# Kernel tuning notes

Measured on AMD Instinct MI355X. Metric: run time of the kernel, lower is better.

## Reference

```python
import jax, jax.numpy as jnp
import numpy as np

N = 10000; E = 320000
DIM = 176; ATT = 16; SH_HEADS = 16; TH = 4; NH = SH_HEADS + TH; VD = DIM // SH_HEADS
LMAX = 3; NSPH = (LMAX + 1) ** 2; ZDIM = 16; RDIM = 16
RSTART = 0.8; CUT = 5.0; NLAYERS = 2


def _ln(x):
    mu = jnp.mean(x, axis=-1, keepdims=True)
    dx = x - mu
    var = jnp.mean(dx ** 2, axis=-1, keepdims=True)
    return dx * (1e-6 + var) ** (-0.5)


def _sph(v):
    # real spherical harmonics up to l=3, unnormalized overall scale, [E,16]
    x, y, z = v[..., 0], v[..., 1], v[..., 2]
    s3 = np.float32(np.sqrt(3.0)); s15 = np.float32(np.sqrt(15.0))
    c1 = np.float32(np.sqrt(5.0 / 8.0)); c2 = np.float32(np.sqrt(3.0 / 8.0))
    x2, y2, z2 = x * x, y * y, z * z
    return jnp.stack([
        jnp.ones_like(x),
        x, y, z,
        s3 * x * y, s3 * y * z, 0.5 * (3.0 * z2 - 1.0), s3 * x * z, 0.5 * s3 * (x2 - y2),
        c1 * y * (3.0 * x2 - y2), s15 * x * y * z, c2 * y * (5.0 * z2 - 1.0),
        0.5 * z * (5.0 * z2 - 3.0), c2 * x * (5.0 * z2 - 1.0),
        0.5 * s15 * z * (x2 - y2), c1 * x * (x2 - 3.0 * y2),
    ], axis=-1)


def setup_inputs() -> dict:
    key = jax.random.key(0)
    ks = jax.random.split(key, 32)

    def rn(k, shape):
        fan_in = shape[0] if len(shape) > 1 else shape[0]
        return jax.random.normal(k, shape, dtype=jnp.float32) / np.float32(np.sqrt(shape[0]))

    species = jax.random.randint(ks[0], (N,), 0, 64)
    edge_src = jax.random.randint(ks[1], (E,), 0, N)
    edge_dst = jax.random.randint(ks[2], (E,), 0, N)
    distances = RSTART + (CUT - RSTART) * jax.random.uniform(ks[3], (E,), dtype=jnp.float32)
    raw = jax.random.normal(ks[4], (E, 3), dtype=jnp.float32)
    dirn = raw / jnp.linalg.norm(raw, axis=-1, keepdims=True)
    vec = dirn * distances[:, None]
    switch = 0.5 * (jnp.cos(jnp.pi * distances / CUT) + 1.0)

    inp = {
        'species': species, 'distances': distances, 'switch': switch,
        'edge_src': edge_src, 'edge_dst': edge_dst, 'vec': vec,
        'z_table': jax.random.normal(ks[5], (64, ZDIM), dtype=jnp.float32),
        'w_species': rn(ks[6], (ZDIM, DIM)),
        'pos_w1_0': rn(ks[7], (RDIM, 2 * ATT)), 'pos_b1_0': jnp.zeros((2 * ATT,), jnp.float32),
        'pos_w2_0': rn(ks[8], (2 * ATT, ATT)), 'pos_b2_0': jnp.zeros((ATT,), jnp.float32),
        'wq_0': rn(ks[9], (DIM, NH * ATT)), 'wk_0': rn(ks[10], (DIM, NH * ATT)),
        'wv_0': rn(ks[11], (DIM, SH_HEADS * VD)),
        'upd_w_0': rn(ks[12], (2 * DIM, DIM)), 'upd_b_0': jnp.zeros((DIM,), jnp.float32),
        'pos_w1_1': rn(ks[13], (RDIM + TH * (LMAX + 1), 2 * ATT)), 'pos_b1_1': jnp.zeros((2 * ATT,), jnp.float32),
        'pos_w2_1': rn(ks[14], (2 * ATT, ATT)), 'pos_b2_1': jnp.zeros((ATT,), jnp.float32),
        'wq_1': rn(ks[15], (DIM, NH * ATT)), 'wk_1': rn(ks[16], (DIM, NH * ATT)),
        'wv_1': rn(ks[17], (DIM, SH_HEADS * VD)),
        'upd_w_1': rn(ks[18], (2 * DIM, DIM)), 'upd_b_1': jnp.zeros((DIM,), jnp.float32),
    }
    return inp


def reference(species, distances, switch, edge_src, edge_dst, vec,
              z_table, w_species,
              pos_w1_0, pos_b1_0, pos_w2_0, pos_b2_0, wq_0, wk_0, wv_0, upd_w_0, upd_b_0,
              pos_w1_1, pos_b1_1, pos_w2_1, pos_b2_1, wq_1, wk_1, wv_1, upd_w_1, upd_b_1):
    Nn = species.shape[0]
    Zi = z_table[species]                      # [N, ZDIM] species encoding
    xi = _ln(Zi @ w_species)                   # [N, DIM]

    vhat = vec / distances[:, None]
    Yij = _sph(vhat)                           # [E, NSPH]
    ls = np.repeat(np.arange(LMAX + 1), 2 * np.arange(LMAX + 1) + 1)
    parity = jnp.asarray(((-1.0) ** ls).astype(np.float32))  # [NSPH]

    centers = jnp.linspace(RSTART, CUT, RDIM, dtype=jnp.float32)
    sigma = np.float32((CUT - RSTART) / (RDIM - 1))
    radial = jnp.exp(-(((distances[:, None] - centers) / sigma) ** 2))  # [E, RDIM]

    Vi = jnp.zeros((Nn, TH, NSPH), jnp.float32)
    pos = [(pos_w1_0, pos_b1_0, pos_w2_0, pos_b2_0), (pos_w1_1, pos_b1_1, pos_w2_1, pos_b2_1)]
    att = [(wq_0, wk_0, wv_0, upd_w_0, upd_b_0), (wq_1, wk_1, wv_1, upd_w_1, upd_b_1)]
    inv_sqrt_d = np.float32(1.0 / np.sqrt(ATT))

    for layer in range(NLAYERS):
        pw1, pb1, pw2, pb2 = pos[layer]
        wq, wk, wv, uw, ub = att[layer]
        if layer == 0:
            ur = radial
        else:
            # tensor relative positional features: [E, TH, NSPH]
            xij2 = (Vi[edge_dst] + (parity * Vi)[edge_src]) * Yij[:, None, :]
            us = [xij2[:, :, l * l:(l + 1) * (l + 1)].sum(axis=-1) for l in range(LMAX + 1)]
            ur = jnp.concatenate([radial] + us, axis=-1)
        w = jax.nn.swish(ur @ pw1 + pb1) @ pw2 + pb2     # [E, ATT] positional encoding
        q = (xi @ wq).reshape(Nn, NH, ATT)
        k = (xi @ wk).reshape(Nn, NH, ATT)
        # multiplicative relative positional attention coefficients [E, NH]
        aij = jnp.einsum('ehd,ed->eh', q[edge_dst] * k[edge_src], w) * (switch[:, None] * inv_sqrt_d)
        a_s, a_t = aij[:, :SH_HEADS], aij[:, SH_HEADS:]
        v = (xi @ wv).reshape(Nn, SH_HEADS, VD)
        mi = jax.ops.segment_sum(a_s[:, :, None] * v[edge_src], edge_dst, num_segments=Nn)  # [N,SH,VD]
        Vi = Vi + jax.ops.segment_sum(
            a_t[:, :, None] * (Yij[:, None, :] + parity * Vi[edge_src]), edge_dst, num_segments=Nn)
        ui = jnp.concatenate([xi, mi.reshape(Nn, -1)], axis=-1)
        xi = _ln(xi + ui @ uw + ub)
    return xi
```

## Files before the change

### kernel.cpp

```cpp
#include <hip/hip_runtime.h>
#include <hip/hip_bf16.h>
#include <math.h>

#define N_NODES 10000
#define N_PAD   10048
#define N_EDGES 320000
#define DIM     176
#define ATT     16
#define SH_HEADS 16
#define THH     4
#define NH      20
#define VD      11
#define ZDIM    16
#define RDIM    16
#define QK_W    (NH*ATT)
#define QKV_W   816
#define UI_W    (2*DIM)
#define KQ      192
#define SIGINV  3.5714285714285716f
#define RSTEP   0.28f

typedef unsigned short ushort_t;
typedef __attribute__((ext_vector_type(8))) short bf16x8;
typedef __attribute__((ext_vector_type(4))) float f32x4;


__device__ __forceinline__ ushort_t f2bf(float f) {
    __hip_bfloat16 b = __float2bfloat16(f);
    return *(ushort_t*)&b;
}

__device__ __forceinline__ float bf2f(ushort_t u) {
    return __uint_as_float(((unsigned)u) << 16);
}

__device__ __forceinline__ void sph16(float x, float y, float z, float* Y) {
    const float s3  = 1.7320508075688772f;
    const float s15 = 3.872983346207417f;
    const float c1  = 0.7905694150420949f;
    const float c2  = 0.6123724356957945f;
    float x2 = x*x, y2 = y*y, z2 = z*z;
    Y[0]  = 1.0f;
    Y[1]  = x;
    Y[2]  = y;
    Y[3]  = z;
    Y[4]  = s3 * x * y;
    Y[5]  = s3 * y * z;
    Y[6]  = 0.5f * (3.0f * z2 - 1.0f);
    Y[7]  = s3 * x * z;
    Y[8]  = 0.5f * s3 * (x2 - y2);
    Y[9]  = c1 * y * (3.0f * x2 - y2);
    Y[10] = s15 * x * y * z;
    Y[11] = c2 * y * (5.0f * z2 - 1.0f);
    Y[12] = 0.5f * z * (5.0f * z2 - 3.0f);
    Y[13] = c2 * x * (5.0f * z2 - 1.0f);
    Y[14] = 0.5f * s15 * z * (x2 - y2);
    Y[15] = c1 * x * (x2 - 3.0f * y2);
}

__device__ __forceinline__ void unpack8(const uint4 u, float* f) {
    f[0] = __uint_as_float(u.x << 16);
    f[1] = __uint_as_float(u.x & 0xffff0000u);
    f[2] = __uint_as_float(u.y << 16);
    f[3] = __uint_as_float(u.y & 0xffff0000u);
    f[4] = __uint_as_float(u.z << 16);
    f[5] = __uint_as_float(u.z & 0xffff0000u);
    f[6] = __uint_as_float(u.w << 16);
    f[7] = __uint_as_float(u.w & 0xffff0000u);
}


__global__ __launch_bounds__(256) void k_deg(const int* edst, int* deg) {
    int e = blockIdx.x * 256 + threadIdx.x;
    if (e < N_EDGES) atomicAdd(&deg[edst[e]], 1);
}

__global__ __launch_bounds__(1024) void k_scan1(const int* deg, int* incl, int* bsum) {
    __shared__ int sd[1024];
    int b = blockIdx.x, tid = threadIdx.x;
    int gi = b * 1024 + tid;
    int v = (gi < N_NODES) ? deg[gi] : 0;
    sd[tid] = v;
    __syncthreads();
    for (int s = 1; s < 1024; s <<= 1) {
        int add = (tid >= s) ? sd[tid - s] : 0;
        __syncthreads();
        sd[tid] += add;
        __syncthreads();
    }
    if (gi < N_NODES) incl[gi] = sd[tid];
    if (tid == 1023) bsum[b] = sd[1023];
}

__global__ __launch_bounds__(1024) void k_scan3(const int* deg, const int* incl, const int* bsum,
                                                int* off, int* cursor) {
    __shared__ int bpre_s;
    int b = blockIdx.x, tid = threadIdx.x;
    if (tid == 0) {
        int acc = 0;
        for (int k = 0; k < b; k++) acc += bsum[k];
        bpre_s = acc;
    }
    __syncthreads();
    int gi = b * 1024 + tid;
    if (gi < N_NODES) {
        int e = bpre_s + incl[gi];
        off[gi + 1] = e;
        cursor[gi]  = e - deg[gi];
    }
    if (gi == 0) off[0] = 0;
}

__global__ __launch_bounds__(256) void k_scatter_reorder(const int* esrc, const int* edst,
        const float* dist, const float* swit, const float* vec, int* cursor,
        int* src_c, int* dst_c, float* dist_c, float* sc_c, float* Yf) {
    int e = blockIdx.x * 256 + threadIdx.x;
    if (e >= N_EDGES) return;
    int t_ = edst[e];
    int p = atomicAdd(&cursor[t_], 1);
    float d = dist[e];
    float inv = 1.0f / d;
    float vx = vec[(size_t)e*3 + 0] * inv;
    float vy = vec[(size_t)e*3 + 1] * inv;
    float vz = vec[(size_t)e*3 + 2] * inv;
    src_c[p]  = esrc[e];
    dst_c[p]  = t_;
    dist_c[p] = d;
    sc_c[p]   = swit[e] * 0.25f;
    float Y[16];
    sph16(vx, vy, vz, Y);
    #pragma unroll
    for (int m = 0; m < 16; m += 4)
        *(float4*)&Yf[(size_t)p * 16 + m] = make_float4(Y[m], Y[m+1], Y[m+2], Y[m+3]);
}


__device__ __forceinline__ void prep_qkv_body(int bid, int tid, const float* wq,
        const float* wk, const float* wv, ushort_t* Wtq) {
    int id = bid * 256 + tid;
    if (id >= 832 * KQ) return;
    int n = id / KQ, k = id - (id / KQ) * KQ;
    float v = 0.0f;
    if (k < DIM && n < QKV_W)
        v = (n < 320) ? wq[k * 320 + n] : (n < 640) ? wk[k * 320 + (n - 320)]
                                                    : wv[k * DIM + (n - 640)];
    Wtq[id] = f2bf(v);
}

__device__ __forceinline__ void prep_upd_body(int bid, int tid, const float* uw, ushort_t* Wtu) {
    int id = bid * 256 + tid;
    if (id >= 192 * UI_W) return;
    int n = id / UI_W, k = id - (id / UI_W) * UI_W;
    float v = (n < DIM) ? uw[k * DIM + n] : 0.0f;
    Wtu[id] = f2bf(v);
}

__device__ __forceinline__ void prep_mlp_body(int bid, int tid, const float* pw1,
        const float* pw2, ushort_t* w1T, ushort_t* w2T, int K1) {
    int id = bid * 256 + tid;
    if (id < 1024) {
        int n = id >> 5, k = id & 31;
        w1T[n * 32 + k] = (k < K1) ? f2bf(pw1[k * 32 + n]) : 0;
    } else if (id < 1536) {
        int id2 = id - 1024;
        int n = id2 >> 5, k = id2 & 31;
        w2T[n * 32 + k] = f2bf(pw2[k * 16 + n]);
    }
}

__global__ __launch_bounds__(256) void k_prep_all(
        const float* wq0, const float* wk0, const float* wv0, ushort_t* Wtq0,
        const float* wq1, const float* wk1, const float* wv1, ushort_t* Wtq1,
        const float* uw0, ushort_t* Wtu0, const float* uw1, ushort_t* Wtu1,
        const float* pw1_0, const float* pw2_0, ushort_t* w1T0, ushort_t* w2T0,
        const float* pw1_1, const float* pw2_1, ushort_t* w1T1, ushort_t* w2T1) {
    int bid = blockIdx.x, tid = threadIdx.x;
    if (bid < 624)        prep_qkv_body(bid,        tid, wq0, wk0, wv0, Wtq0);
    else if (bid < 1248)  prep_qkv_body(bid - 624,  tid, wq1, wk1, wv1, Wtq1);
    else if (bid < 1512)  prep_upd_body(bid - 1248, tid, uw0, Wtu0);
    else if (bid < 1776)  prep_upd_body(bid - 1512, tid, uw1, Wtu1);
    else if (bid < 1782)  prep_mlp_body(bid - 1776, tid, pw1_0, pw2_0, w1T0, w2T0, 16);
    else if (bid < 1788)  prep_mlp_body(bid - 1782, tid, pw1_1, pw2_1, w1T1, w2T1, 32);
}


template<int KCHUNKS, int OMODE>
__global__ __launch_bounds__(256) void k_gemm(const ushort_t* __restrict__ A, int sA,
                                              const ushort_t* __restrict__ Bt, int sB,
                                              void* __restrict__ Cv, int sC, int M, int N,
                                              ushort_t* __restrict__ qh,
                                              ushort_t* __restrict__ kh,
                                              ushort_t* __restrict__ vh) {
    __shared__ ushort_t As[64 * 40];
    __shared__ ushort_t Bs[64 * 40];
    int tid  = threadIdx.x;
    int m0   = blockIdx.y * 64, n0 = blockIdx.x * 64;
    int w    = tid >> 6, lane = tid & 63, quad = lane >> 4, c16 = lane & 15;
    int arow = tid >> 2, aseg = tid & 3;
    f32x4 acc[4] = {};
    for (int kc = 0; kc < KCHUNKS; kc++) {
        int k0 = kc * 32;
        *(uint4*)&As[arow * 40 + aseg * 8] =
            *(const uint4*)&A[(size_t)(m0 + arow) * sA + k0 + aseg * 8];
        *(uint4*)&Bs[arow * 40 + aseg * 8] =
            *(const uint4*)&Bt[(size_t)(n0 + arow) * sB + k0 + aseg * 8];
        __syncthreads();
        bf16x8 a = *(const bf16x8*)&As[(w * 16 + c16) * 40 + quad * 8];
        #pragma unroll
        for (int t = 0; t < 4; t++) {
            bf16x8 b = *(const bf16x8*)&Bs[(t * 16 + c16) * 40 + quad * 8];
            acc[t] = __builtin_amdgcn_mfma_f32_16x16x32_bf16(a, b, acc[t], 0, 0, 0);
        }
        __syncthreads();
    }
    #pragma unroll
    for (int t = 0; t < 4; t++) {
        #pragma unroll
        for (int r = 0; r < 4; r++) {
            int row = m0 + w * 16 + quad * 4 + r;
            int col = n0 + t * 16 + c16;
            if (row < M && col < N) {
                if (OMODE == 1) {
                    ushort_t bv = f2bf(acc[t][r]);
                    if (col < 320)      qh[(size_t)row * QK_W + col] = bv;
                    else if (col < 640) kh[(size_t)row * QK_W + (col - 320)] = bv;
                    else                vh[(size_t)row * DIM  + (col - 640)] = bv;
                } else {
                    ((float*)Cv)[(size_t)row * sC + col] = acc[t][r];
                }
            }
        }
    }
}


__global__ __launch_bounds__(256) void k_node_init(const int* species, const float* z_table,
                                                   const float* wsp, float* xi,
                                                   ushort_t* xib, ushort_t* cxm) {
    __shared__ float zs[16 * ZDIM];
    __shared__ float yt[16 * DIM];
    __shared__ float red[256];
    __shared__ float mus[16], rstds[16];
    int base = blockIdx.x * 16;
    int tid  = threadIdx.x;
    { int n = tid >> 4, kk = tid & 15;
      zs[tid] = z_table[species[base + n] * ZDIM + kk]; }
    __syncthreads();
    int c = tid;
    if (c < DIM) {
        float acc[16];
        #pragma unroll
        for (int n = 0; n < 16; n++) acc[n] = 0.0f;
        for (int kk = 0; kk < ZDIM; kk++) {
            float w = wsp[kk * DIM + c];
            #pragma unroll
            for (int n = 0; n < 16; n++) acc[n] += zs[n * ZDIM + kk] * w;
        }
        #pragma unroll
        for (int n = 0; n < 16; n++) yt[n * DIM + c] = acc[n];
    }
    __syncthreads();
    { int n2 = tid >> 4, j = tid & 15;
      float s = 0.0f;
      for (int c2 = j; c2 < DIM; c2 += 16) s += yt[n2 * DIM + c2];
      red[tid] = s; }
    __syncthreads();
    if (tid < 16) { float s = 0; for (int j = 0; j < 16; j++) s += red[tid * 16 + j]; mus[tid] = s / (float)DIM; }
    __syncthreads();
    { int n2 = tid >> 4, j = tid & 15;
      float mu = mus[n2], s = 0.0f;
      for (int c2 = j; c2 < DIM; c2 += 16) { float d = yt[n2 * DIM + c2] - mu; s += d * d; }
      red[tid] = s; }
    __syncthreads();
    if (tid < 16) { float s = 0; for (int j = 0; j < 16; j++) s += red[tid * 16 + j]; rstds[tid] = rsqrtf(s / (float)DIM + 1e-6f); }
    __syncthreads();
    if (c < DIM) {
        #pragma unroll
        for (int n = 0; n < 16; n++) {
            float val = (yt[n * DIM + c] - mus[n]) * rstds[n];
            xi[(size_t)(base + n) * DIM + c] = val;
            ushort_t bv = f2bf(val);
            xib[(size_t)(base + n) * KQ + c]   = bv;
            cxm[(size_t)(base + n) * UI_W + c] = bv;
        }
    } else if (c < KQ) {
        #pragma unroll
        for (int n = 0; n < 16; n++) xib[(size_t)(base + n) * KQ + c] = 0;
    }
}


template<bool L0>
__global__ __launch_bounds__(256) void k_edge(const float* dist_c, const float* sc_c,
        const int* src_c, const int* dst_c, const float* Yf, const ushort_t* Vih,
        const ushort_t* qh, const ushort_t* kh,
        const ushort_t* w1T, const float* pb1, const ushort_t* w2T, const float* pb2,
        ushort_t* aijh) {
    __shared__ ushort_t urS[64 * 40];
    __shared__ ushort_t Ht[4][16 * 40];
    __shared__ float    wdS[64 * 17];
    __shared__ ushort_t aS[NH][64];
    int tid  = threadIdx.x;
    int w    = tid >> 6, lane = tid & 63, quad = lane >> 4, c16 = lane & 15;
    int eb   = blockIdx.x * 64;

    int le = tid >> 2, part = tid & 3;
    int ie = eb + le;
    int sE = src_c[ie], tE = dst_c[ie];

    if (!L0) {
        int e  = tid & 63, tp = tid >> 6;
        int i  = eb + e;
        float d = dist_c[i];
        ushort_t ur4[4];
        #pragma unroll
        for (int r0 = 0; r0 < 4; r0++) {
            int r = tp * 4 + r0;
            float cc = 0.8f + (float)r * RSTEP;
            float uu = (d - cc) * SIGINV;
            ur4[r0] = f2bf(__expf(-uu * uu));
        }
        *(uint2*)&urS[e * 40 + tp * 4] = *(uint2*)ur4;
        float Y[16];
        #pragma unroll
        for (int m = 0; m < 16; m += 4) {
            float4 y = *(const float4*)&Yf[(size_t)i * 16 + m];
            Y[m] = y.x; Y[m+1] = y.y; Y[m+2] = y.z; Y[m+3] = y.w;
        }
        int s = src_c[i], t_ = dst_c[i];
        const uint4* vd4 = (const uint4*)(Vih + (size_t)t_ * 64);
        const uint4* vs4 = (const uint4*)(Vih + (size_t)s  * 64);
        int th = tp;
        float fd[16], fs[16];
        unpack8(vd4[2*th],   fd);     unpack8(vd4[2*th+1], fd+8);
        unpack8(vs4[2*th],   fs);     unpack8(vs4[2*th+1], fs+8);
        float us0 = (fd[0] + fs[0]) * Y[0];
        float us1 = 0.0f, us2 = 0.0f, us3 = 0.0f;
        #pragma unroll
        for (int m = 1; m < 4; m++)  us1 += (fd[m] - fs[m]) * Y[m];
        #pragma unroll
        for (int m = 4; m < 9; m++)  us2 += (fd[m] + fs[m]) * Y[m];
        #pragma unroll
        for (int m = 9; m < 16; m++) us3 += (fd[m] - fs[m]) * Y[m];
        urS[e * 40 + 16 + 0 * 4 + th] = f2bf(us0);
        urS[e * 40 + 16 + 1 * 4 + th] = f2bf(us1);
        urS[e * 40 + 16 + 2 * 4 + th] = f2bf(us2);
        urS[e * 40 + 16 + 3 * 4 + th] = f2bf(us3);
        __syncthreads();
    }

    uint4 kr[10];
    {
        const uint4* kseg = (const uint4*)(kh + (size_t)sE * QK_W) + part * 10;
        #pragma unroll
        for (int j = 0; j < 10; j++) kr[j] = kseg[j];
    }

    {
        int e0 = eb + w * 16;
        bf16x8 a1;
        if (L0) {
            float d = dist_c[e0 + c16];
            #pragma unroll
            for (int j = 0; j < 8; j++) {
                int r = quad * 8 + j;
                float v = 0.0f;
                if (r < 16) { float cc = 0.8f + (float)r * RSTEP; float uu = (d - cc) * SIGINV; v = __expf(-uu * uu); }
                a1[j] = (short)f2bf(v);
            }
        } else {
            a1 = *(const bf16x8*)&urS[(w * 16 + c16) * 40 + quad * 8];
        }
        bf16x8 b0 = *(const bf16x8*)&w1T[c16 * 32 + quad * 8];
        bf16x8 b1 = *(const bf16x8*)&w1T[(16 + c16) * 32 + quad * 8];
        f32x4 acc0 = {}, acc1 = {};
        acc0 = __builtin_amdgcn_mfma_f32_16x16x32_bf16(a1, b0, acc0, 0, 0, 0);
        acc1 = __builtin_amdgcn_mfma_f32_16x16x32_bf16(a1, b1, acc1, 0, 0, 0);
        float bb0 = pb1[c16], bb1 = pb1[c16 + 16];
        #pragma unroll
        for (int r = 0; r < 4; r++) {
            int er = quad * 4 + r;
            float h0 = acc0[r] + bb0; h0 = h0 / (1.0f + __expf(-h0));
            float h1 = acc1[r] + bb1; h1 = h1 / (1.0f + __expf(-h1));
            Ht[w][er * 40 + c16]      = f2bf(h0);
            Ht[w][er * 40 + 16 + c16] = f2bf(h1);
        }
        __syncthreads();
        bf16x8 a2 = *(const bf16x8*)&Ht[w][c16 * 40 + quad * 8];
        bf16x8 b2 = *(const bf16x8*)&w2T[c16 * 32 + quad * 8];
        f32x4 acc2 = {};
        acc2 = __builtin_amdgcn_mfma_f32_16x16x32_bf16(a2, b2, acc2, 0, 0, 0);
        float bb2 = pb2[c16];
        #pragma unroll
        for (int r = 0; r < 4; r++) {
            int er = quad * 4 + r;
            wdS[(w * 16 + er) * 17 + c16] = (acc2[r] + bb2) * sc_c[e0 + er];
        }
    }
    __syncthreads();

    {
        float wd[16];
        #pragma unroll
        for (int p = 0; p < 16; p++) wd[p] = wdS[le * 17 + p];
        const uint4* q4 = (const uint4*)(qh + (size_t)tE * QK_W) + part * 10;
        #pragma unroll
        for (int j = 0; j < 5; j++) {
            int h = part * 5 + j;
            float qa[8], qb[8], ka[8], kb[8];
            unpack8(q4[2*j],   qa); unpack8(q4[2*j+1], qb);
            unpack8(kr[2*j],   ka); unpack8(kr[2*j+1], kb);
            float acc = 0.0f;
            #pragma unroll
            for (int dd = 0; dd < 8; dd++) acc += qa[dd] * ka[dd] * wd[dd];
            #pragma unroll
            for (int dd = 0; dd < 8; dd++) acc += qb[dd] * kb[dd] * wd[8 + dd];
            aS[h][le] = f2bf(acc);
        }
    }
    __syncthreads();
    {
        const uint* aSw = (const uint*)aS;
        for (int idx = tid; idx < NH * 32; idx += 256) {
            int h = idx >> 5, w2 = idx & 31;
            *(uint*)(aijh + (size_t)h * N_EDGES + eb + w2 * 2) = aSw[h * 32 + w2];
        }
    }
}


__device__ __forceinline__ void mi_step(int i, int c0, bool f1, bool f2,
        const int* src_c, const ushort_t* aA, const ushort_t* aB, const ushort_t* vh,
        float& acc0, float& acc1, float& acc2, float& acc3) {
    int s0 = src_c[i];
    uint2 v0 = *(const uint2*)(vh + (size_t)s0 * DIM + c0);
    float a00 = bf2f(aA[i]), a0B = bf2f(aB[i]);
    float g01 = f1 ? a0B : a00, g02 = f2 ? a0B : a00;
    acc0 += a00 * __uint_as_float(v0.x << 16);
    acc1 += g01 * __uint_as_float(v0.x & 0xffff0000u);
    acc2 += g02 * __uint_as_float(v0.y << 16);
    acc3 += a0B * __uint_as_float(v0.y & 0xffff0000u);
}

__device__ __forceinline__ void mi_wave(int n, int lane, const int* off, const int* src_c,
        const ushort_t* aijh, const ushort_t* vh, ushort_t* cxm) {
    if (lane >= 44) return;
    int c0 = lane * 4;
    int hA = c0 / VD;
    int hB = (c0 + 3) / VD;
    bool f1 = ((c0 + 1) / VD) != hA;
    bool f2 = ((c0 + 2) / VD) != hA;
    const ushort_t* aA = aijh + (size_t)hA * N_EDGES;
    const ushort_t* aB = aijh + (size_t)hB * N_EDGES;
    int start = off[n], end = off[n + 1];
    float acc0 = 0, acc1 = 0, acc2 = 0, acc3 = 0;
    int cnt = end - start;
    int i = start;

#define MI_ACC(vv, av, bv) { \
    float aa = bf2f(av), ab = bf2f(bv); \
    float g1 = f1 ? ab : aa, g2 = f2 ? ab : aa; \
    acc0 += aa * __uint_as_float((vv).x << 16); \
    acc1 += g1 * __uint_as_float((vv).x & 0xffff0000u); \
    acc2 += g2 * __uint_as_float((vv).y << 16); \
    acc3 += ab * __uint_as_float((vv).y & 0xffff0000u); }

    if (cnt >= 4) {
        int iend = start + (cnt & ~3);
        int s0 = src_c[i], s1 = src_c[i+1], s2 = src_c[i+2], s3 = src_c[i+3];
        uint2 v0 = *(const uint2*)(vh + (size_t)s0 * DIM + c0);
        uint2 v1 = *(const uint2*)(vh + (size_t)s1 * DIM + c0);
        uint2 v2 = *(const uint2*)(vh + (size_t)s2 * DIM + c0);
        uint2 v3 = *(const uint2*)(vh + (size_t)s3 * DIM + c0);
        ushort_t pA0 = aA[i], pA1 = aA[i+1], pA2 = aA[i+2], pA3 = aA[i+3];
        ushort_t pB0 = aB[i], pB1 = aB[i+1], pB2 = aB[i+2], pB3 = aB[i+3];
        for (i += 4; i + 4 <= iend; i += 4) {
            int t0 = src_c[i], t1 = src_c[i+1], t2 = src_c[i+2], t3 = src_c[i+3];
            uint2 w0 = *(const uint2*)(vh + (size_t)t0 * DIM + c0);
            uint2 w1 = *(const uint2*)(vh + (size_t)t1 * DIM + c0);
            uint2 w2 = *(const uint2*)(vh + (size_t)t2 * DIM + c0);
            uint2 w3 = *(const uint2*)(vh + (size_t)t3 * DIM + c0);
            ushort_t qA0 = aA[i], qA1 = aA[i+1], qA2 = aA[i+2], qA3 = aA[i+3];
            ushort_t qB0 = aB[i], qB1 = aB[i+1], qB2 = aB[i+2], qB3 = aB[i+3];
            MI_ACC(v0, pA0, pB0); MI_ACC(v1, pA1, pB1);
            MI_ACC(v2, pA2, pB2); MI_ACC(v3, pA3, pB3);
            v0 = w0; v1 = w1; v2 = w2; v3 = w3;
            pA0 = qA0; pA1 = qA1; pA2 = qA2; pA3 = qA3;
            pB0 = qB0; pB1 = qB1; pB2 = qB2; pB3 = qB3;
        }
        MI_ACC(v0, pA0, pB0); MI_ACC(v1, pA1, pB1);
        MI_ACC(v2, pA2, pB2); MI_ACC(v3, pA3, pB3);
    }
    for (; i < end; i++)
        mi_step(i, c0, f1, f2, src_c, aA, aB, vh, acc0, acc1, acc2, acc3);
#undef MI_ACC
    ushort_t o[4] = {f2bf(acc0), f2bf(acc1), f2bf(acc2), f2bf(acc3)};
    *(uint2*)(cxm + (size_t)n * UI_W + DIM + c0) = *(uint2*)o;
}

__device__ __forceinline__ void vi_wave(int n, int lane, const int* off,
        const float* Yf, const ushort_t* aijh, ushort_t* Vih) {
    int th = lane >> 4, sm = lane & 15;
    const ushort_t* ah = aijh + (size_t)(SH_HEADS + th) * N_EDGES;
    int start = off[n], end = off[n + 1];
    float acc = 0.0f;
    int cnt = end - start;
    int i = start;
    if (cnt >= 4) {
        int iend = start + (cnt & ~3);
        float a0 = bf2f(ah[i]),   y0 = Yf[(size_t)i * 16 + sm];
        float a1 = bf2f(ah[i+1]), y1 = Yf[(size_t)(i+1) * 16 + sm];
        float a2 = bf2f(ah[i+2]), y2 = Yf[(size_t)(i+2) * 16 + sm];
        float a3 = bf2f(ah[i+3]), y3 = Yf[(size_t)(i+3) * 16 + sm];
        for (i += 4; i + 4 <= iend; i += 4) {
            float b0 = bf2f(ah[i]),   z0 = Yf[(size_t)i * 16 + sm];
            float b1 = bf2f(ah[i+1]), z1 = Yf[(size_t)(i+1) * 16 + sm];
            float b2 = bf2f(ah[i+2]), z2 = Yf[(size_t)(i+2) * 16 + sm];
            float b3 = bf2f(ah[i+3]), z3 = Yf[(size_t)(i+3) * 16 + sm];
            acc += a0 * y0 + a1 * y1 + a2 * y2 + a3 * y3;
            a0 = b0; a1 = b1; a2 = b2; a3 = b3;
            y0 = z0; y1 = z1; y2 = z2; y3 = z3;
        }
        acc += a0 * y0 + a1 * y1 + a2 * y2 + a3 * y3;
    }
    for (; i < end; i++)
        acc += bf2f(ah[i]) * Yf[(size_t)i * 16 + sm];
    Vih[(size_t)n * 64 + lane] = f2bf(acc);
}

__global__ __launch_bounds__(256) void k_agg0(const int* off, const int* src_c,
        const float* Yf, const ushort_t* aijh, const ushort_t* vh,
        ushort_t* cxm, ushort_t* Vih) {
    int wid  = blockIdx.x * 4 + (threadIdx.x >> 6);
    int lane = threadIdx.x & 63;
    if (wid < N_NODES)
        mi_wave(wid, lane, off, src_c, aijh, vh, cxm);
    else
        vi_wave(wid - N_NODES, lane, off, Yf, aijh, Vih);
}

__global__ __launch_bounds__(256) void k_agg1(const int* off, const int* src_c,
        const ushort_t* aijh, const ushort_t* vh, ushort_t* cxm) {
    int wid  = blockIdx.x * 4 + (threadIdx.x >> 6);
    int lane = threadIdx.x & 63;
    mi_wave(wid, lane, off, src_c, aijh, vh, cxm);
}


__global__ __launch_bounds__(256) void k_lnfinal(const float* yg, const float* xi,
        const float* ub, float* xo, ushort_t* xib, ushort_t* cxm) {
    __shared__ float yt[16 * DIM];
    __shared__ float red[256];
    __shared__ float mus[16], rstds[16];
    int base = blockIdx.x * 16;
    int tid  = threadIdx.x;
    for (int idx = tid; idx < 16 * DIM; idx += 256) {
        int n = idx / DIM, c = idx - n * DIM;
        yt[idx] = xi[(size_t)(base + n) * DIM + c]
                + yg[(size_t)(base + n) * DIM + c] + ub[c];
    }
    __syncthreads();
    { int n2 = tid >> 4, j = tid & 15;
      float s = 0.0f;
      for (int c2 = j; c2 < DIM; c2 += 16) s += yt[n2 * DIM + c2];
      red[tid] = s; }
    __syncthreads();
    if (tid < 16) { float s = 0; for (int j = 0; j < 16; j++) s += red[tid * 16 + j]; mus[tid] = s / (float)DIM; }
    __syncthreads();
    { int n2 = tid >> 4, j = tid & 15;
      float mu = mus[n2], s = 0.0f;
      for (int c2 = j; c2 < DIM; c2 += 16) { float d = yt[n2 * DIM + c2] - mu; s += d * d; }
      red[tid] = s; }
    __syncthreads();
    if (tid < 16) { float s = 0; for (int j = 0; j < 16; j++) s += red[tid * 16 + j]; rstds[tid] = rsqrtf(s / (float)DIM + 1e-6f); }
    __syncthreads();
    int c = tid;
    if (c < DIM) {
        #pragma unroll
        for (int n = 0; n < 16; n++) {
            float val = (yt[n * DIM + c] - mus[n]) * rstds[n];
            xo[(size_t)(base + n) * DIM + c] = val;
            ushort_t bv = f2bf(val);
            xib[(size_t)(base + n) * KQ + c]   = bv;
            cxm[(size_t)(base + n) * UI_W + c] = bv;
        }
    } else if (c < KQ) {
        #pragma unroll
        for (int n = 0; n < 16; n++) xib[(size_t)(base + n) * KQ + c] = 0;
    }
}


extern "C" void kernel_launch(void* const* d_in, const int* in_sizes, int n_in,
                              void* d_out, int out_size, void* d_ws, size_t ws_size,
                              hipStream_t stream) {
    const int*   species = (const int*)  d_in[0];
    const float* dist    = (const float*)d_in[1];
    const float* swit    = (const float*)d_in[2];
    const int*   esrc    = (const int*)  d_in[3];
    const int*   edst    = (const int*)  d_in[4];
    const float* vec     = (const float*)d_in[5];
    const float* z_table = (const float*)d_in[6];
    const float* wsp     = (const float*)d_in[7];
    const float* pw1_0 = (const float*)d_in[8],  *pb1_0 = (const float*)d_in[9];
    const float* pw2_0 = (const float*)d_in[10], *pb2_0 = (const float*)d_in[11];
    const float* wq0 = (const float*)d_in[12], *wk0 = (const float*)d_in[13];
    const float* wv0 = (const float*)d_in[14], *uw0 = (const float*)d_in[15];
    const float* ub0 = (const float*)d_in[16];
    const float* pw1_1 = (const float*)d_in[17], *pb1_1 = (const float*)d_in[18];
    const float* pw2_1 = (const float*)d_in[19], *pb2_1 = (const float*)d_in[20];
    const float* wq1 = (const float*)d_in[21], *wk1 = (const float*)d_in[22];
    const float* wv1 = (const float*)d_in[23], *uw1 = (const float*)d_in[24];
    const float* ub1 = (const float*)d_in[25];
    float* out = (float*)d_out;

    char* p = (char*)d_ws;
    auto alloc = [&](size_t bytes) -> char* {
        char* r = p;
        p += (bytes + 255) & ~(size_t)255;
        return r;
    };
    int* deg    = (int*)alloc((size_t)N_NODES * 4);
    int* incl   = (int*)alloc((size_t)N_NODES * 4);
    int* bsum   = (int*)alloc(64);
    int* off    = (int*)alloc((size_t)(N_NODES + 1) * 4);
    int* cursor = (int*)alloc((size_t)N_NODES * 4);
    int*   src_c  = (int*)  alloc((size_t)N_EDGES * 4);
    int*   dst_c  = (int*)  alloc((size_t)N_EDGES * 4);
    float* dist_c = (float*)alloc((size_t)N_EDGES * 4);
    float* sc_c   = (float*)alloc((size_t)N_EDGES * 4);
    float* Yf     = (float*)alloc((size_t)N_EDGES * 16 * 4);
    float* xiA  = (float*)alloc((size_t)N_NODES * DIM * 4);
    float* xiB  = (float*)alloc((size_t)N_NODES * DIM * 4);
    ushort_t* xib  = (ushort_t*)alloc((size_t)N_PAD * KQ * 2);
    ushort_t* cxm  = (ushort_t*)alloc((size_t)N_PAD * UI_W * 2);
    ushort_t* qh   = (ushort_t*)alloc((size_t)N_NODES * QK_W * 2);
    ushort_t* kh   = (ushort_t*)alloc((size_t)N_NODES * QK_W * 2);
    ushort_t* vh   = (ushort_t*)alloc((size_t)N_NODES * DIM * 2);
    float* ybuf    = (float*)alloc((size_t)N_NODES * DIM * 4);
    ushort_t* Wtq0 = (ushort_t*)alloc((size_t)832 * KQ * 2);
    ushort_t* Wtq1 = (ushort_t*)alloc((size_t)832 * KQ * 2);
    ushort_t* Wtu0 = (ushort_t*)alloc((size_t)192 * UI_W * 2);
    ushort_t* Wtu1 = (ushort_t*)alloc((size_t)192 * UI_W * 2);
    ushort_t* w1T0 = (ushort_t*)alloc((size_t)32 * 32 * 2);
    ushort_t* w2T0 = (ushort_t*)alloc((size_t)16 * 32 * 2);
    ushort_t* w1T1 = (ushort_t*)alloc((size_t)32 * 32 * 2);
    ushort_t* w2T1 = (ushort_t*)alloc((size_t)16 * 32 * 2);
    ushort_t* Vih  = (ushort_t*)alloc((size_t)N_NODES * 64 * 2);
    ushort_t* aijh = (ushort_t*)alloc((size_t)N_EDGES * NH * 2);

    const int NB_E  = (N_EDGES + 255) / 256;
    const int NB_F  = N_EDGES / 64;
    const int NB_T  = N_NODES / 16;
    const dim3 GRID_QKV(13, 157);
    const dim3 GRID_UPD(3, 157);

    hipMemsetAsync(deg, 0, (size_t)N_NODES * 4, stream);
    k_deg<<<NB_E, 256, 0, stream>>>(edst, deg);
    k_scan1<<<10, 1024, 0, stream>>>(deg, incl, bsum);
    k_scan3<<<10, 1024, 0, stream>>>(deg, incl, bsum, off, cursor);
    k_scatter_reorder<<<NB_E, 256, 0, stream>>>(esrc, edst, dist, swit, vec, cursor,
                                                src_c, dst_c, dist_c, sc_c, Yf);

    k_prep_all<<<1788, 256, 0, stream>>>(wq0, wk0, wv0, Wtq0, wq1, wk1, wv1, Wtq1,
                                         uw0, Wtu0, uw1, Wtu1,
                                         pw1_0, pw2_0, w1T0, w2T0,
                                         pw1_1, pw2_1, w1T1, w2T1);

    k_node_init<<<NB_T, 256, 0, stream>>>(species, z_table, wsp, xiA, xib, cxm);

    k_gemm<6, 1><<<GRID_QKV, 256, 0, stream>>>(xib, KQ, Wtq0, KQ, nullptr, 0,
                                               N_NODES, QKV_W, qh, kh, vh);
    k_edge<true><<<NB_F, 256, 0, stream>>>(dist_c, sc_c, src_c, dst_c, Yf, Vih,
                                           qh, kh, w1T0, pb1_0, w2T0, pb2_0, aijh);
    k_agg0<<<5000, 256, 0, stream>>>(off, src_c, Yf, aijh, vh, cxm, Vih);
    k_gemm<11, 0><<<GRID_UPD, 256, 0, stream>>>(cxm, UI_W, Wtu0, UI_W, ybuf, DIM,
                                                N_NODES, DIM, nullptr, nullptr, nullptr);
    k_lnfinal<<<NB_T, 256, 0, stream>>>(ybuf, xiA, ub0, xiB, xib, cxm);

    k_gemm<6, 1><<<GRID_QKV, 256, 0, stream>>>(xib, KQ, Wtq1, KQ, nullptr, 0,
                                               N_NODES, QKV_W, qh, kh, vh);
    k_edge<false><<<NB_F, 256, 0, stream>>>(dist_c, sc_c, src_c, dst_c, Yf, Vih,
                                            qh, kh, w1T1, pb1_1, w2T1, pb2_1, aijh);
    k_agg1<<<2500, 256, 0, stream>>>(off, src_c, aijh, vh, cxm);
    k_gemm<11, 0><<<GRID_UPD, 256, 0, stream>>>(cxm, UI_W, Wtu1, UI_W, ybuf, DIM,
                                                N_NODES, DIM, nullptr, nullptr, nullptr);
    k_lnfinal<<<NB_T, 256, 0, stream>>>(ybuf, xiB, ub1, out, xib, cxm);
}
```

Measured before the change: 386.6 us.

## Replace atomic-cursor edge scatter with rank-based permutation and gathered CSR build

The degree-count kernel now records each edge's atomic rank, which removes the second atomic pass over the cursors. A new permutation kernel places each edge index at its CSR slot. A build kernel then walks CSR positions in order, gathering the edge attributes and writing the sorted arrays and spherical harmonics with coalesced stores instead of scattered ones. The cost is one extra kernel launch plus the rank and perm buffers, and the gathered reads from the original edge arrays are random.

Measured after the change: 384.3 us. Within noise of the previous version (-0.6%).

```diff
diff --git a/kernel.cpp b/kernel.cpp
--- a/kernel.cpp
+++ b/kernel.cpp
@@ -70,9 +70,9 @@
 }
 
 
-__global__ __launch_bounds__(256) void k_deg(const int* edst, int* deg) {
+__global__ __launch_bounds__(256) void k_deg(const int* edst, int* deg, int* rank) {
     int e = blockIdx.x * 256 + threadIdx.x;
-    if (e < N_EDGES) atomicAdd(&deg[edst[e]], 1);
+    if (e < N_EDGES) rank[e] = atomicAdd(&deg[edst[e]], 1);
 }
 
 __global__ __launch_bounds__(1024) void k_scan1(const int* deg, int* incl, int* bsum) {
@@ -93,7 +93,7 @@
 }
 
 __global__ __launch_bounds__(1024) void k_scan3(const int* deg, const int* incl, const int* bsum,
-                                                int* off, int* cursor) {
+                                                int* off) {
     __shared__ int bpre_s;
     int b = blockIdx.x, tid = threadIdx.x;
     if (tid == 0) {
@@ -104,29 +104,39 @@
     __syncthreads();
     int gi = b * 1024 + tid;
     if (gi < N_NODES) {
-        int e = bpre_s + incl[gi];
-        off[gi + 1] = e;
-        cursor[gi]  = e - deg[gi];
+        off[gi + 1] = bpre_s + incl[gi];
     }
     if (gi == 0) off[0] = 0;
 }
 
-__global__ __launch_bounds__(256) void k_scatter_reorder(const int* esrc, const int* edst,
-        const float* dist, const float* swit, const float* vec, int* cursor,
-        int* src_c, int* dst_c, float* dist_c, float* sc_c, float* Yf) {
+__global__ __launch_bounds__(256) void k_perm(const int* edst, const int* rank,
+                                              const int* off, int* perm) {
     int e = blockIdx.x * 256 + threadIdx.x;
     if (e >= N_EDGES) return;
+    perm[off[edst[e]] + rank[e]] = e;
+}
+
+__global__ __launch_bounds__(256) void k_build(const int* __restrict__ perm,
+        const int* __restrict__ esrc, const int* __restrict__ edst,
+        const float* __restrict__ dist, const float* __restrict__ swit,
+        const float* __restrict__ vec,
+        int* src_c, int* dst_c, float* dist_c, float* sc_c, float* Yf) {
+    int p = blockIdx.x * 256 + threadIdx.x;
+    if (p >= N_EDGES) return;
+    int e  = perm[p];
+    int s  = esrc[e];
     int t_ = edst[e];
-    int p = atomicAdd(&cursor[t_], 1);
-    float d = dist[e];
+    float d  = dist[e];
+    float sw = swit[e];
+    float vx = vec[(size_t)e*3 + 0];
+    float vy = vec[(size_t)e*3 + 1];
+    float vz = vec[(size_t)e*3 + 2];
     float inv = 1.0f / d;
-    float vx = vec[(size_t)e*3 + 0] * inv;
-    float vy = vec[(size_t)e*3 + 1] * inv;
-    float vz = vec[(size_t)e*3 + 2] * inv;
-    src_c[p]  = esrc[e];
+    vx *= inv; vy *= inv; vz *= inv;
+    src_c[p]  = s;
     dst_c[p]  = t_;
     dist_c[p] = d;
-    sc_c[p]   = swit[e] * 0.25f;
+    sc_c[p]   = sw * 0.25f;
     float Y[16];
     sph16(vx, vy, vz, Y);
     #pragma unroll
@@ -624,7 +634,8 @@
     int* incl   = (int*)alloc((size_t)N_NODES * 4);
     int* bsum   = (int*)alloc(64);
     int* off    = (int*)alloc((size_t)(N_NODES + 1) * 4);
-    int* cursor = (int*)alloc((size_t)N_NODES * 4);
+    int* rank   = (int*)alloc((size_t)N_EDGES * 4);
+    int* perm   = (int*)alloc((size_t)N_EDGES * 4);
     int*   src_c  = (int*)  alloc((size_t)N_EDGES * 4);
     int*   dst_c  = (int*)  alloc((size_t)N_EDGES * 4);
     float* dist_c = (float*)alloc((size_t)N_EDGES * 4);
@@ -656,11 +667,12 @@
     const dim3 GRID_UPD(3, 157);
 
     hipMemsetAsync(deg, 0, (size_t)N_NODES * 4, stream);
-    k_deg<<<NB_E, 256, 0, stream>>>(edst, deg);
+    k_deg<<<NB_E, 256, 0, stream>>>(edst, deg, rank);
     k_scan1<<<10, 1024, 0, stream>>>(deg, incl, bsum);
-    k_scan3<<<10, 1024, 0, stream>>>(deg, incl, bsum, off, cursor);
-    k_scatter_reorder<<<NB_E, 256, 0, stream>>>(esrc, edst, dist, swit, vec, cursor,
-                                                src_c, dst_c, dist_c, sc_c, Yf);
+    k_scan3<<<10, 1024, 0, stream>>>(deg, incl, bsum, off);
+    k_perm<<<NB_E, 256, 0, stream>>>(edst, rank, off, perm);
+    k_build<<<NB_E, 256, 0, stream>>>(perm, esrc, edst, dist, swit, vec,
+                                      src_c, dst_c, dist_c, sc_c, Yf);
 
     k_prep_all<<<1788, 256, 0, stream>>>(wq0, wk0, wv0, Wtq0, wq1, wk1, wv1, Wtq1,
                                          uw0, Wtu0, uw1, Wtu1,
```
